# Optimization experiments

Measured on AMD Instinct MI355X. Metric: run time of the kernel, lower is better.

Reference implementation:

```python
import jax, jax.numpy as jnp
import numpy as np

STRIDE = 1
PADDING = 1

def setup_inputs() -> dict:
    key = jax.random.key(0)
    k1, k2 = jax.random.split(key)
    x = jax.random.normal(k1, (16, 64, 224, 224), dtype=jnp.float32)
    weight = jax.random.normal(k2, (64, 64, 3, 3), dtype=jnp.float32)
    return {"x": x, "weight": weight}

def reference(x, weight):
    # Module's per-tap shift-and-add loop is exactly cross-correlation conv2d:
    # weight indexed [out, in, kh, kw] with ZeroPad2d(padding) and given stride.
    return jax.lax.conv_general_dilated(
        x, weight,
        window_strides=(STRIDE, STRIDE),
        padding=((PADDING, PADDING), (PADDING, PADDING)),
        dimension_numbers=("NCHW", "OIHW", "NCHW"),
    )
```

## Files before the change

### kernel.cpp

```cpp
#include <hip/hip_runtime.h>


#define HH 224
#define WW 224
#define CHW (HH * WW)
#define PLANE 4352
#define NSLOT 18

typedef short bf16x8 __attribute__((ext_vector_type(8)));
typedef float f32x16 __attribute__((ext_vector_type(16)));

__device__ __forceinline__ unsigned short f2bf(float f) {
    union { float f; unsigned int u; } v; v.f = f;
    unsigned int u = v.u;
    return (unsigned short)((u + 0x7fffu + ((u >> 16) & 1u)) >> 16);
}

#define SGB  __builtin_amdgcn_sched_group_barrier
#define MFMA __builtin_amdgcn_mfma_f32_32x32x16_bf16

__global__ void wprep_kernel(const float* __restrict__ wgt, unsigned short* __restrict__ wb) {
    const int i = blockIdx.x * 256 + threadIdx.x;
    if (i >= 36864) return;
    const int j   = i & 7;
    const int oc  = (i >> 3) & 63;
    const int g   = (i >> 9) & 1;
    const int ks  = i >> 10;
    const int tap = ks >> 2;
    const int c   = (ks & 3) * 16 + g * 8 + j;
    wb[i] = f2bf(wgt[(oc * 64 + c) * 9 + tap]);
}

#define MMA_CQ(dw, cq, WFU) do {                                              \
    const int off_ = (((cq) * 32 + g16) ^ swz_);                              \
    const bf16x8 B0 = *(const bf16x8*)(ldsB + sl0 + wb_ + off_);              \
    const bf16x8 B1 = *(const bf16x8*)(ldsB + sl1 + wb_ + off_);              \
    const bf16x8 B2 = *(const bf16x8*)(ldsB + sl2 + wb_ + off_);              \
    const bf16x8 B3 = *(const bf16x8*)(ldsB + sl3 + wb_ + off_);              \
    const bf16x8 B4 = *(const bf16x8*)(ldsB + sl4 + wb_ + off_);              \
    const bf16x8 B5 = *(const bf16x8*)(ldsB + sl5 + wb_ + off_);              \
    a0 = MFMA(wfrag[(dw)*4 + (cq)], B0, a0, 0, 0, 0);                         \
    a1 = MFMA(wfrag[(dw)*4 + (cq)], B1, a1, 0, 0, 0);                         \
    a2 = MFMA(wfrag[(dw)*4 + (cq)], B2, a2, 0, 0, 0);                         \
    a3 = MFMA(wfrag[(dw)*4 + (cq)], B3, a3, 0, 0, 0);                         \
    a0 = MFMA(wfrag[12 + (dw)*4 + (cq)], B1, a0, 0, 0, 0);                    \
    a1 = MFMA(wfrag[12 + (dw)*4 + (cq)], B2, a1, 0, 0, 0);                    \
    a2 = MFMA(wfrag[12 + (dw)*4 + (cq)], B3, a2, 0, 0, 0);                    \
    a3 = MFMA(wfrag[12 + (dw)*4 + (cq)], B4, a3, 0, 0, 0);                    \
    a0 = MFMA(WFU, B2, a0, 0, 0, 0);                                          \
    a1 = MFMA(WFU, B3, a1, 0, 0, 0);                                          \
    a2 = MFMA(WFU, B4, a2, 0, 0, 0);                                          \
    a3 = MFMA(WFU, B5, a3, 0, 0, 0);                                          \
    SGB(0x100, 6, 0); SGB(0x008, 12, 0);                                      \
} while (0)

#define SECTION(dw, cqp, WFU0, WFU1, WFLD0, WFLD1, ldw, lcqp) do {            \
    WFLD0 = *(const bf16x8*)(wlane + ((6 + (ldw))*4 + 2*(lcqp)    ) * 1024);  \
    WFLD1 = *(const bf16x8*)(wlane + ((6 + (ldw))*4 + 2*(lcqp) + 1) * 1024);  \
    const int wl_  = s + (dw);                                                \
    const int swz_ = (wl_ & 7) << 4;                                          \
    const int wb_  = wl_ * 128;                                               \
    MMA_CQ(dw, 2*(cqp),     WFU0);                                            \
    MMA_CQ(dw, 2*(cqp) + 1, WFU1);                                            \
} while (0)

#define STI(k) do { if (st) {                                                 \
    const int r_ = h + 9 + (k);                                               \
    const bool ok_ = (r_ < HH);                                               \
    _Pragma("unroll")                                                         \
    for (int j = 0; j < 8; ++j) pv[j] = ok_ ? pxm[j*CHW + r_*WW] : 0.f;       \
    if (tid >= 240) {                                                         \
        const bool okh_ = ok_ && hokw;                                        \
        _Pragma("unroll")                                                     \
        for (int j = 0; j < 8; ++j) hv[j] = okh_ ? pxh[j*CHW + r_*WW] : 0.f;  \
    } } } while (0)

#define STW(k) do { if (st) {                                                 \
    int sw_ = slw + (k); if (sw_ >= NSLOT) sw_ -= NSLOT;                      \
    bf16x8 f_;                                                                \
    _Pragma("unroll")                                                         \
    for (int j = 0; j < 8; ++j) f_[j] = (short)f2bf(pv[j]);                   \
    *(bf16x8*)(ldsB + sw_ * PLANE + lom) = f_;                                \
    if (tid >= 240) {                                                         \
        bf16x8 fh_;                                                           \
        _Pragma("unroll")                                                     \
        for (int j = 0; j < 8; ++j) fh_[j] = (short)f2bf(hv[j]);              \
        *(bf16x8*)(ldsB + sw_ * PLANE + loh) = fh_;                           \
    } } } while (0)

__global__ __launch_bounds__(256, 2)
void conv3x3_mfma(const float* __restrict__ x, const unsigned short* __restrict__ wb,
                  float* __restrict__ out) {
    __shared__ __align__(16) unsigned short lds[NSLOT * 34 * 64];
    char* ldsB = (char*)lds;

    const int tid  = threadIdx.x;
    const int lane = tid & 63;
    const int wv   = tid >> 6;
    const int och  = wv & 1;
    const int rg4  = wv >> 1;
    const int s    = lane & 31;
    const int g    = lane >> 5;
    const int g16  = g * 16;

    const int bid = blockIdx.x;
    const int n   = bid / 28;
    const int rem = bid % 28;
    const int ws  = rem / 4;
    const int hc  = rem % 4;
    const int wbase = ws * 32;
    const int h0    = hc * 56;

    const unsigned short* wlane = wb + g * 512 + (och * 32 + s) * 8;
    bf16x8 wfrag[24];
#pragma unroll
    for (int ks = 0; ks < 24; ++ks)
        wfrag[ks] = *(const bf16x8*)(wlane + ks * 1024);
    bf16x8 wfA0 = *(const bf16x8*)(wlane + 24 * 1024);
    bf16x8 wfA1 = *(const bf16x8*)(wlane + 25 * 1024);
    bf16x8 wfB0 = {}, wfB1 = {};

    for (int p = tid; p < 10 * 272; p += 256) {
        const int rrel = p / 272;
        const int q  = p % 272;
        const int c8 = q / 34;
        const int wl = q % 34;
        const int r  = h0 - 1 + rrel;
        const int gw = wbase - 1 + wl;
        bf16x8 f = {};
        if (r >= 0 && r < HH && gw >= 0 && gw < WW) {
            const float* px = x + (n * 64 + c8 * 8) * CHW + r * WW + gw;
#pragma unroll
            for (int j = 0; j < 8; ++j) f[j] = (short)f2bf(px[j * CHW]);
        }
        *(bf16x8*)(ldsB + ((r + NSLOT) % NSLOT) * PLANE + wl * 128
                   + ((c8 * 16) ^ ((wl & 7) << 4))) = f;
    }

    const int c8m = tid >> 5;
    const int wlm = 1 + (tid & 31);
    const float* pxm = x + (n * 64 + c8m * 8) * CHW + (wbase + (tid & 31));
    const int lom = wlm * 128 + ((c8m * 16) ^ ((wlm & 7) << 4));
    const int c8h = lane & 7;
    const int wlh = ((lane >> 3) & 1) * 33;
    const int gwh = wbase - 1 + wlh;
    const bool hokw = (gwh >= 0 && gwh < WW);
    const float* pxh = x + (n * 64 + c8h * 8) * CHW + gwh;
    const int loh = wlh * 128 + ((c8h * 16) ^ ((wlh & 7) << 4));

    __syncthreads();

#pragma unroll 1
    for (int it = 0; it < 7; ++it) {
        const int h  = h0 + 8 * it;
        const int hb = h + 4 * rg4;
        const bool st = (it < 6);
        const int slw = (h + 9) % NSLOT;

        int t_ = (hb - 1 + NSLOT) % NSLOT;
        const int sl0 = t_ * PLANE; t_ = (t_ + 1 == NSLOT) ? 0 : t_ + 1;
        const int sl1 = t_ * PLANE; t_ = (t_ + 1 == NSLOT) ? 0 : t_ + 1;
        const int sl2 = t_ * PLANE; t_ = (t_ + 1 == NSLOT) ? 0 : t_ + 1;
        const int sl3 = t_ * PLANE; t_ = (t_ + 1 == NSLOT) ? 0 : t_ + 1;
        const int sl4 = t_ * PLANE; t_ = (t_ + 1 == NSLOT) ? 0 : t_ + 1;
        const int sl5 = t_ * PLANE;

        float pv[8], hv[8];
        f32x16 a0 = {}, a1 = {}, a2 = {}, a3 = {};

        STI(0); SECTION(0, 0, wfA0, wfA1, wfB0, wfB1, 0, 1); STW(0);
        STI(1); SECTION(0, 1, wfB0, wfB1, wfA0, wfA1, 1, 0); STW(1);
        STI(2); SECTION(1, 0, wfA0, wfA1, wfB0, wfB1, 1, 1); STW(2);
        STI(3); SECTION(1, 1, wfB0, wfB1, wfA0, wfA1, 2, 0); STW(3);
        STI(4); SECTION(2, 0, wfA0, wfA1, wfB0, wfB1, 2, 1); STW(4);
        STI(5); SECTION(2, 1, wfB0, wfB1, wfA0, wfA1, 0, 0); STW(5);

        float* po = out + (n * 64 + och * 32 + 4 * g) * CHW + hb * WW + wbase + s;
        STI(6);
#pragma unroll
        for (int rg = 0; rg < 16; ++rg) {
            const int o_ = ((rg & 3) + 8 * (rg >> 2)) * CHW;
            po[o_]      = a0[rg];
            po[o_ + WW] = a1[rg];
        }
        STW(6); STI(7);
#pragma unroll
        for (int rg = 0; rg < 16; ++rg) {
            const int o_ = ((rg & 3) + 8 * (rg >> 2)) * CHW;
            po[o_ + 2 * WW] = a2[rg];
            po[o_ + 3 * WW] = a3[rg];
        }
        STW(7);

        __syncthreads();
    }
}

extern "C" void kernel_launch(void* const* d_in, const int* in_sizes, int n_in,
                              void* d_out, int out_size, void* d_ws, size_t ws_size,
                              hipStream_t stream) {
    const float* x   = (const float*)d_in[0];
    const float* wgt = (const float*)d_in[1];
    float* out       = (float*)d_out;
    unsigned short* wbuf = (unsigned short*)d_ws;

    wprep_kernel<<<dim3(144), dim3(256), 0, stream>>>(wgt, wbuf);
    conv3x3_mfma<<<dim3(448), dim3(256), 0, stream>>>(x, wbuf, out);
}
```

Baseline: 177.1 us.

## Vectorize halo row staging loads and deepen prefetch to four rows ahead

Row staging now loads pairs of adjacent pixels with float2 over four channels per thread instead of eight scalar channel loads. The halo columns are spread across all threads rather than handled by the last 16 threads. Four rows are fetched into registers before the MMA sections begin, so global latency overlaps several compute sections rather than one. In exchange it uses more VGPRs, which risks the 2-blocks-per-CU occupancy target, and LDS writes shrink to 8-byte stores.

```diff
diff --git a/kernel.cpp b/kernel.cpp
--- a/kernel.cpp
+++ b/kernel.cpp
@@ -7,6 +7,7 @@
 #define PLANE 4352
 #define NSLOT 18
 
+typedef short bf16x4 __attribute__((ext_vector_type(4)));
 typedef short bf16x8 __attribute__((ext_vector_type(8)));
 typedef float f32x16 __attribute__((ext_vector_type(16)));
 
@@ -64,28 +65,30 @@
     MMA_CQ(dw, 2*(cqp) + 1, WFU1);                                            \
 } while (0)
 
-#define STI(k) do { if (st) {                                                 \
+#define STIS(k, P) do { if (st) {                                             \
     const int r_ = h + 9 + (k);                                               \
     const bool ok_ = (r_ < HH);                                               \
     _Pragma("unroll")                                                         \
-    for (int j = 0; j < 8; ++j) pv[j] = ok_ ? pxm[j*CHW + r_*WW] : 0.f;       \
-    if (tid >= 240) {                                                         \
-        const bool okh_ = ok_ && hokw;                                        \
+    for (int i = 0; i < 4; ++i) {                                             \
+        if (ok_) P[i] = *(const float2*)(pxm + i * CHW + r_ * WW);            \
+        else { P[i].x = 0.f; P[i].y = 0.f; }                                  \
+    } } } while (0)
+
+#define STWS(k, P) do { if (st) {                                             \
+    int sw_ = slw + (k); if (sw_ >= NSLOT) sw_ -= NSLOT;                      \
+    bf16x4 lo_, hi_;                                                          \
+    _Pragma("unroll")                                                         \
+    for (int i = 0; i < 4; ++i) {                                             \
+        lo_[i] = (short)f2bf(P[i].x);                                         \
+        hi_[i] = (short)f2bf(P[i].y);                                         \
+    }                                                                         \
+    *(bf16x4*)(ldsB + sw_ * PLANE + wA * 128 + (cg8 ^ swzA)) = lo_;           \
+    *(bf16x4*)(ldsB + sw_ * PLANE + wB * 128 + (cg8 ^ swzB)) = hi_;           \
+    if (hk == (k)) {                                                          \
+        bf16x4 hh_;                                                           \
         _Pragma("unroll")                                                     \
-        for (int j = 0; j < 8; ++j) hv[j] = okh_ ? pxh[j*CHW + r_*WW] : 0.f;  \
-    } } } while (0)
-
-#define STW(k) do { if (st) {                                                 \
-    int sw_ = slw + (k); if (sw_ >= NSLOT) sw_ -= NSLOT;                      \
-    bf16x8 f_;                                                                \
-    _Pragma("unroll")                                                         \
-    for (int j = 0; j < 8; ++j) f_[j] = (short)f2bf(pv[j]);                   \
-    *(bf16x8*)(ldsB + sw_ * PLANE + lom) = f_;                                \
-    if (tid >= 240) {                                                         \
-        bf16x8 fh_;                                                           \
-        _Pragma("unroll")                                                     \
-        for (int j = 0; j < 8; ++j) fh_[j] = (short)f2bf(hv[j]);              \
-        *(bf16x8*)(ldsB + sw_ * PLANE + loh) = fh_;                           \
+        for (int i = 0; i < 4; ++i) hh_[i] = (short)f2bf(hv[i]);              \
+        *(bf16x4*)(ldsB + sw_ * PLANE + hwl * 128 + (hcg8 ^ hswz)) = hh_;     \
     } } } while (0)
 
 __global__ __launch_bounds__(256, 2)
@@ -137,16 +140,24 @@
                    + ((c8 * 16) ^ ((wl & 7) << 4))) = f;
     }
 
-    const int c8m = tid >> 5;
-    const int wlm = 1 + (tid & 31);
-    const float* pxm = x + (n * 64 + c8m * 8) * CHW + (wbase + (tid & 31));
-    const int lom = wlm * 128 + ((c8m * 16) ^ ((wlm & 7) << 4));
-    const int c8h = lane & 7;
-    const int wlh = ((lane >> 3) & 1) * 33;
-    const int gwh = wbase - 1 + wlh;
-    const bool hokw = (gwh >= 0 && gwh < WW);
-    const float* pxh = x + (n * 64 + c8h * 8) * CHW + gwh;
-    const int loh = wlh * 128 + ((c8h * 16) ^ ((wlh & 7) << 4));
+    const int wp  = tid & 15;
+    const int cg  = tid >> 4;
+    const int cg8 = cg * 8;
+    const int wA  = 1 + 2 * wp;
+    const int wB  = 2 + 2 * wp;
+    const int swzA = (wA & 7) << 4;
+    const int swzB = (wB & 7) << 4;
+    const float* pxm = x + (n * 64 + 4 * cg) * CHW + (wbase + 2 * wp);
+
+    const int hk   = tid >> 5;
+    const int hs   = tid & 31;
+    const int hcg  = hs & 15;
+    const int hcg8 = hcg * 8;
+    const int hwl  = (hs >> 4) ? 33 : 0;
+    const int hswz = (hwl & 7) << 4;
+    const int ghw  = wbase - 1 + hwl;
+    const bool hokw = (ghw >= 0 && ghw < WW);
+    const float* pxh = x + (n * 64 + 4 * hcg) * CHW + ghw;
 
     __syncthreads();
 
@@ -165,32 +176,41 @@
         const int sl4 = t_ * PLANE; t_ = (t_ + 1 == NSLOT) ? 0 : t_ + 1;
         const int sl5 = t_ * PLANE;
 
-        float pv[8], hv[8];
+        float2 p0[4], p1[4], p2[4], p3[4];
+        float hv[4];
         f32x16 a0 = {}, a1 = {}, a2 = {}, a3 = {};
 
-        STI(0); SECTION(0, 0, wfA0, wfA1, wfB0, wfB1, 0, 1); STW(0);
-        STI(1); SECTION(0, 1, wfB0, wfB1, wfA0, wfA1, 1, 0); STW(1);
-        STI(2); SECTION(1, 0, wfA0, wfA1, wfB0, wfB1, 1, 1); STW(2);
-        STI(3); SECTION(1, 1, wfB0, wfB1, wfA0, wfA1, 2, 0); STW(3);
-        STI(4); SECTION(2, 0, wfA0, wfA1, wfB0, wfB1, 2, 1); STW(4);
-        STI(5); SECTION(2, 1, wfB0, wfB1, wfA0, wfA1, 0, 0); STW(5);
+        STIS(0, p0); STIS(1, p1); STIS(2, p2); STIS(3, p3);
+        if (st) {
+            const int rh_ = h + 9 + hk;
+            const bool ok_ = (rh_ < HH) && hokw;
+#pragma unroll
+            for (int i = 0; i < 4; ++i) hv[i] = ok_ ? pxh[i * CHW + rh_ * WW] : 0.f;
+        }
+        __builtin_amdgcn_sched_barrier(0);
+
+        SECTION(0, 0, wfA0, wfA1, wfB0, wfB1, 0, 1); STWS(0, p0); STIS(4, p0);
+        SECTION(0, 1, wfB0, wfB1, wfA0, wfA1, 1, 0); STWS(1, p1); STIS(5, p1);
+        SECTION(1, 0, wfA0, wfA1, wfB0, wfB1, 1, 1); STWS(2, p2); STIS(6, p2);
+        SECTION(1, 1, wfB0, wfB1, wfA0, wfA1, 2, 0); STWS(3, p3); STIS(7, p3);
+        SECTION(2, 0, wfA0, wfA1, wfB0, wfB1, 2, 1); STWS(4, p0);
+        SECTION(2, 1, wfB0, wfB1, wfA0, wfA1, 0, 0); STWS(5, p1);
 
         float* po = out + (n * 64 + och * 32 + 4 * g) * CHW + hb * WW + wbase + s;
-        STI(6);
 #pragma unroll
         for (int rg = 0; rg < 16; ++rg) {
             const int o_ = ((rg & 3) + 8 * (rg >> 2)) * CHW;
             po[o_]      = a0[rg];
             po[o_ + WW] = a1[rg];
         }
-        STW(6); STI(7);
+        STWS(6, p2);
 #pragma unroll
         for (int rg = 0; rg < 16; ++rg) {
             const int o_ = ((rg & 3) + 8 * (rg >> 2)) * CHW;
             po[o_ + 2 * WW] = a2[rg];
             po[o_ + 3 * WW] = a3[rg];
         }
-        STW(7);
+        STWS(7, p3);
 
         __syncthreads();
     }
```

After: 222.9 us. 25.9% more time.
